# Kernel tuning notes

Hardware: AMD Instinct MI355X
Metric: run time of the kernel (lower is better)

The kernel has to match this reference:

```python
import jax, jax.numpy as jnp
import numpy as np

EPSILON = 0.01            # params.epsilon (cluster precision regularizer)
GAMMA = 0.005             # params.gamma (outlier/uniform component weight)
FIX_CLUSTER_POS_ITER = 1  # params.fix_cluster_pos_iter


def _sqdist(TVs, X):
    # TVs: (M, 3, N) transformed points, X: (K, 3) cluster means -> (M, N, K)
    return ((TVs ** 2).sum(1)[:, :, None]
            + (X ** 2).sum(1)[None, None, :]
            - 2.0 * jnp.einsum('mdn,kd->mnk', TVs, X))


def setup_inputs() -> dict:
    key = jax.random.key(0)
    kV, kX, kQ = jax.random.split(key, 3)
    M, N, K = 8, 8192, 256
    Vs = jax.random.normal(kV, (M, 3, N), dtype=jnp.float32)      # 3D point clouds
    X0 = jax.random.normal(kX, (K, 3), dtype=jnp.float32)         # init cluster means (sphere init)
    Q0 = 0.1 + 0.2 * jax.random.uniform(kQ, (K,), dtype=jnp.float32)  # init cluster precisions
    return {"Vs": Vs, "X0": X0, "Q0": Q0, "num_iters": 6}


def reference(Vs, X0, Q0, num_iters):
    M, _, N = Vs.shape
    K = X0.shape[0]
    dtype = Vs.dtype

    # mean_init: init_R = I, init_t = -mean(V) per view
    t0 = -Vs.mean(axis=2, keepdims=True)          # (M, 3, 1)
    TVs = Vs + t0
    beta = GAMMA * jnp.mean(Q0) ** 1.5            # get_default_beta(Q, gamma)

    X, Q = X0, Q0
    ds = _sqdist(TVs, X)                          # (M, N, K)
    R = jnp.broadcast_to(jnp.eye(3, dtype=dtype), (M, 3, 3))
    t = t0[:, :, 0]

    for i in range(num_iters):
        if i != num_iters - 1:  # detach everything except backprop_iter = [last]
            X = jax.lax.stop_gradient(X)
            Q = jax.lax.stop_gradient(Q)
            ds = jax.lax.stop_gradient(ds)

        # E-step: soft posteriors with uniform outlier component beta
        ap = jnp.exp(-0.5 * ds * Q) * Q ** 1.5    # (M, N, K); priors = 1, pyz_feature = 1
        a = ap / (ap.sum(axis=-1, keepdims=True) + beta)

        # M-step: weighted sufficient statistics
        L = a.sum(axis=1)                                   # (M, K)
        W = jnp.einsum('mdn,mnk->mdk', Vs, a) * Q           # (M, 3, K)
        mW = W.sum(axis=-1)                                 # (M, 3)
        b = L * Q                                           # (M, K)
        mX = jnp.einsum('mk,kd->md', b, X)                  # (M, 3)
        z = b.sum(axis=-1)                                  # (M,)

        # P = (W @ X)^T - mX mW^T / z  : 3x3 weighted cross-covariance per view
        P = (jnp.einsum('mdk,ke->med', W, X)
             - mX[:, :, None] * mW[:, None, :] / z[:, None, None])

        # batched Procrustes: R = U diag(1,1,det(U V^T)) V^T
        U, _, Vt = jnp.linalg.svd(P)
        det = jnp.linalg.det(jnp.einsum('mij,mjk->mik', U, Vt))
        sgn = jnp.concatenate([jnp.ones((M, 2), dtype), det[:, None]], axis=1)
        R = jnp.einsum('mij,mjk->mik', U * sgn[:, None, :], Vt)   # (M, 3, 3)
        t = (mX - jnp.einsum('mij,mj->mi', R, mW)) / z[:, None]   # (M, 3)
        TVs = jnp.einsum('mij,mjn->min', R, Vs) + t[:, :, None]   # (M, 3, N)

        # shared cluster updates (sum over views)
        den = L.sum(axis=0)                                 # (K,)
        if i > FIX_CLUSTER_POS_ITER:
            X = jnp.einsum('mdn,mnk->kd', TVs, a) / den[:, None]
        ds = _sqdist(TVs, X)
        wn = (a * ds).sum(axis=(0, 1))                      # (K,)
        Q = 3.0 * den / (wn + 3.0 * den * EPSILON)

    return TVs, R, t, X
```

## Files before the change

### kernel.cpp

```cpp
#include <hip/hip_runtime.h>
#include <math.h>

#define Mv 8
#define Nv 8192
#define Kv 256
#define BPM 32
#define NBLK (Mv*BPM)
#define NPB (Nv/BPM)
#define NITER 6
#define EPSILON_C 0.01f
#define GAMMA_C 0.005f

#define WS_R     0
#define WS_T     72
#define WS_X     96
#define WS_Q     864
#define WS_BETA  1120
#define WS_ACC   1124
#define AC_STATS 0
#define AC_L     128
#define AC_W     2176
#define AC_H     8320
#define ACCSZ    10368

__device__ __forceinline__ float wave_red_sum(float x) {
  int v;
  float t;
  v = __builtin_bit_cast(int, x);
  t = __builtin_bit_cast(float, __builtin_amdgcn_update_dpp(0, v, 0x111, 0xf, 0xf, true));
  x += t; v = __builtin_bit_cast(int, x);
  t = __builtin_bit_cast(float, __builtin_amdgcn_update_dpp(0, v, 0x112, 0xf, 0xf, true));
  x += t; v = __builtin_bit_cast(int, x);
  t = __builtin_bit_cast(float, __builtin_amdgcn_update_dpp(0, v, 0x114, 0xf, 0xf, true));
  x += t; v = __builtin_bit_cast(int, x);
  t = __builtin_bit_cast(float, __builtin_amdgcn_update_dpp(0, v, 0x118, 0xf, 0xf, true));
  x += t; v = __builtin_bit_cast(int, x);
  t = __builtin_bit_cast(float, __builtin_amdgcn_update_dpp(0, v, 0x142, 0xa, 0xf, false));
  x += t; v = __builtin_bit_cast(int, x);
  t = __builtin_bit_cast(float, __builtin_amdgcn_update_dpp(0, v, 0x143, 0xc, 0xf, false));
  x += t;
  return __builtin_bit_cast(float, __builtin_amdgcn_readlane(__builtin_bit_cast(int, x), 63));
}

__global__ __launch_bounds__(256) void p0_init(const float* __restrict__ Vs,
                                               const float* __restrict__ X0,
                                               const float* __restrict__ Q0,
                                               float* __restrict__ ws) {
  __shared__ float sred[4];
  int tid = threadIdx.x;
  int b = blockIdx.x;
  int wave = tid >> 6, lane = tid & 63;
  if (b < 24) {
    int m = b / 3, d = b % 3;
    const float* src = Vs + (size_t)(m*3 + d) * Nv;
    float s = 0.f;
    for (int n = tid; n < Nv; n += 256) s += src[n];
    s = wave_red_sum(s);
    if (lane == 0) sred[wave] = s;
    __syncthreads();
    if (tid == 0) {
      float tot = sred[0]+sred[1]+sred[2]+sred[3];
      ws[WS_T + m*3 + d] = -tot / (float)Nv;
    }
    if (d == 0 && tid < 9) {
      ws[WS_R + m*9 + tid] = (tid==0||tid==4||tid==8) ? 1.f : 0.f;
    }
  } else {
    float s = (tid < Kv) ? Q0[tid] : 0.f;
    s = wave_red_sum(s);
    if (lane == 0) sred[wave] = s;
    __syncthreads();
    if (tid == 0) {
      float mq = (sred[0]+sred[1]+sred[2]+sred[3]) / (float)Kv;
      ws[WS_BETA] = GAMMA_C * mq * sqrtf(mq);
    }
    if (tid < Kv) ws[WS_Q + tid] = Q0[tid];
    for (int i = tid; i < Kv*3; i += 256) ws[WS_X + i] = X0[i];
    for (int i = tid; i < ACCSZ; i += 256) ws[WS_ACC + i] = 0.f;
  }
}

#define JROTF(app,aqq,apq,apr,aqr, vp0,vp1,vp2, vq0,vq1,vq2) do {           \
    float tau_ = (aqq - app) * __builtin_amdgcn_rcpf(2.0f*apq);             \
    float tt_ = __builtin_amdgcn_rcpf(fabsf(tau_) +                         \
                   __builtin_amdgcn_sqrtf(fmaf(tau_,tau_,1.0f)));           \
    tt_ = (tau_ < 0.0f) ? -tt_ : tt_;                                       \
    tt_ = (apq == 0.0f) ? 0.0f : tt_;                                       \
    float c_ = __builtin_amdgcn_rsqf(fmaf(tt_,tt_,1.0f)), s_ = tt_*c_;      \
    float papq_ = apq;                                                      \
    app = fmaf(-tt_,papq_,app); aqq = fmaf(tt_,papq_,aqq); apq = 0.0f;      \
    float tp_ = apr, tq_ = aqr;                                             \
    apr = c_*tp_ - s_*tq_; aqr = s_*tp_ + c_*tq_;                           \
    tp_=vp0; tq_=vq0; vp0=c_*tp_-s_*tq_; vq0=s_*tp_+c_*tq_;                 \
    tp_=vp1; tq_=vq1; vp1=c_*tp_-s_*tq_; vq1=s_*tp_+c_*tq_;                 \
    tp_=vp2; tq_=vq2; vp2=c_*tp_-s_*tq_; vq2=s_*tp_+c_*tq_;                 \
  } while(0)

#define CSWAP3F(la,lb, a0,a1,a2, b0,b1,b2) do {                             \
    if (la < lb) { float t_;                                                \
      t_=la; la=lb; lb=t_; t_=a0; a0=b0; b0=t_;                             \
      t_=a1; a1=b1; b1=t_; t_=a2; a2=b2; b2=t_; }                           \
  } while(0)

template<int ITPREV>
__device__ __forceinline__ void small_update(const float* __restrict__ acc,
                                             const float* __restrict__ ws,
                                             int tid,
                                             float (*sX)[3], float* sQ,
                                             float (*sR)[9], float (*sT)[3],
                                             float* sTn) {
  const int k = tid;
  float lk[Mv], w0v[Mv], w1v[Mv], w2v[Mv], hk[Mv];
  #pragma unroll
  for (int mm=0;mm<Mv;mm++) {
    lk[mm]  = acc[AC_L + mm*Kv + k];
    w0v[mm] = acc[AC_W + (mm*3+0)*Kv + k];
    w1v[mm] = acc[AC_W + (mm*3+1)*Kv + k];
    w2v[mm] = acc[AC_W + (mm*3+2)*Kv + k];
    hk[mm]  = acc[AC_H + mm*Kv + k];
  }
  float xp0 = 0.f, xp1 = 0.f, xp2 = 0.f;
  if (ITPREV <= 1) {
    xp0 = ws[WS_X + k*3+0]; xp1 = ws[WS_X + k*3+1]; xp2 = ws[WS_X + k*3+2];
  }

  if (tid < Mv) {
    int mm = tid;
    const float* st = acc + AC_STATS + mm*16;
    float s0=st[0], s1=st[1], s2v=st[2], s3=st[3], s4=st[4], s5=st[5],
          s6=st[6], s7=st[7], s8=st[8], s9=st[9], s10=st[10], s11=st[11],
          s12=st[12], s13=st[13], s14=st[14], s15=st[15];
    float z = s0;
    float mX0 = s1, mX1 = s2v, mX2 = s3;
    float mW0 = s4, mW1 = s5, mW2 = s6;
    float iz = __builtin_amdgcn_rcpf(z);
    float P00 = s7  - mX0*mW0*iz;
    float P01 = s8  - mX0*mW1*iz;
    float P02 = s9  - mX0*mW2*iz;
    float P10 = s10 - mX1*mW0*iz;
    float P11 = s11 - mX1*mW1*iz;
    float P12 = s12 - mX1*mW2*iz;
    float P20 = s13 - mX2*mW0*iz;
    float P21 = s14 - mX2*mW1*iz;
    float P22 = s15 - mX2*mW2*iz;
    float a00 = P00*P00 + P10*P10 + P20*P20;
    float a01 = P00*P01 + P10*P11 + P20*P21;
    float a02 = P00*P02 + P10*P12 + P20*P22;
    float a11 = P01*P01 + P11*P11 + P21*P21;
    float a12 = P01*P02 + P11*P12 + P21*P22;
    float a22 = P02*P02 + P12*P12 + P22*P22;
    float v00=1, v01=0, v02=0, v10=0, v11=1, v12=0, v20=0, v21=0, v22=1;
    #pragma unroll 1
    for (int sweep = 0; sweep < 8; sweep++) {
      JROTF(a00,a11,a01, a02,a12, v00,v10,v20, v01,v11,v21);
      JROTF(a00,a22,a02, a01,a12, v00,v10,v20, v02,v12,v22);
      JROTF(a11,a22,a12, a01,a02, v01,v11,v21, v02,v12,v22);
    }
    float l0 = a00, l1 = a11, l2 = a22;
    CSWAP3F(l0,l1, v00,v10,v20, v01,v11,v21);
    CSWAP3F(l1,l2, v01,v11,v21, v02,v12,v22);
    CSWAP3F(l0,l1, v00,v10,v20, v01,v11,v21);
    float detP = P00*(P11*P22-P12*P21) - P01*(P10*P22-P12*P20)
               + P02*(P10*P21-P11*P20);
    float s2d = (detP < 0.0f) ? -1.0f : 1.0f;
    float tiny = 1e-18f*l0 + 1e-30f;
    float w0i = __builtin_amdgcn_rsqf(fmaxf(l0,tiny));
    float w1i = __builtin_amdgcn_rsqf(fmaxf(l1,tiny));
    float w2i = s2d*__builtin_amdgcn_rsqf(fmaxf(l2,tiny));
    float M00 = w0i*v00*v00 + w1i*v01*v01 + w2i*v02*v02;
    float M01 = w0i*v00*v10 + w1i*v01*v11 + w2i*v02*v12;
    float M02 = w0i*v00*v20 + w1i*v01*v21 + w2i*v02*v22;
    float M11 = w0i*v10*v10 + w1i*v11*v11 + w2i*v12*v12;
    float M12 = w0i*v10*v20 + w1i*v11*v21 + w2i*v12*v22;
    float M22 = w0i*v20*v20 + w1i*v21*v21 + w2i*v22*v22;
    float R00n = P00*M00 + P01*M01 + P02*M02;
    float R01n = P00*M01 + P01*M11 + P02*M12;
    float R02n = P00*M02 + P01*M12 + P02*M22;
    float R10n = P10*M00 + P11*M01 + P12*M02;
    float R11n = P10*M01 + P11*M11 + P12*M12;
    float R12n = P10*M02 + P11*M12 + P12*M22;
    float R20n = P20*M00 + P21*M01 + P22*M02;
    float R21n = P20*M01 + P21*M11 + P22*M12;
    float R22n = P20*M02 + P21*M12 + P22*M22;
    float tm0 = (mX0 - (R00n*mW0 + R01n*mW1 + R02n*mW2))*iz;
    float tm1 = (mX1 - (R10n*mW0 + R11n*mW1 + R12n*mW2))*iz;
    float tm2 = (mX2 - (R20n*mW0 + R21n*mW1 + R22n*mW2))*iz;
    sR[mm][0]=R00n; sR[mm][1]=R01n; sR[mm][2]=R02n;
    sR[mm][3]=R10n; sR[mm][4]=R11n; sR[mm][5]=R12n;
    sR[mm][6]=R20n; sR[mm][7]=R21n; sR[mm][8]=R22n;
    sT[mm][0]=tm0; sT[mm][1]=tm1; sT[mm][2]=tm2;
    sTn[mm] = tm0*tm0 + tm1*tm1 + tm2*tm2;
  }
  __syncthreads();
  {
    float den = 0.f, Xn0=0.f, Xn1=0.f, Xn2=0.f, S2=0.f;
    #pragma unroll
    for (int mm=0;mm<Mv;mm++) {
      float r0 = sR[mm][0]*w0v[mm] + sR[mm][1]*w1v[mm] + sR[mm][2]*w2v[mm];
      float r1 = sR[mm][3]*w0v[mm] + sR[mm][4]*w1v[mm] + sR[mm][5]*w2v[mm];
      float r2 = sR[mm][6]*w0v[mm] + sR[mm][7]*w1v[mm] + sR[mm][8]*w2v[mm];
      float tt0 = sT[mm][0], tt1 = sT[mm][1], tt2 = sT[mm][2];
      den += lk[mm];
      Xn0 += r0 + tt0*lk[mm]; Xn1 += r1 + tt1*lk[mm]; Xn2 += r2 + tt2*lk[mm];
      S2  += hk[mm] + 2.f*(tt0*r0+tt1*r1+tt2*r2) + sTn[mm]*lk[mm];
    }
    float x0, x1, x2;
    if (ITPREV > 1) { float inv = __builtin_amdgcn_rcpf(den);
                      x0=Xn0*inv; x1=Xn1*inv; x2=Xn2*inv; }
    else            { x0=xp0; x1=xp1; x2=xp2; }
    float wn = S2 + (x0*x0+x1*x1+x2*x2)*den - 2.f*(x0*Xn0+x1*Xn1+x2*Xn2);
    float qn = 3.f*den / (wn + 3.f*den*EPSILON_C);
    sX[k][0]=x0; sX[k][1]=x1; sX[k][2]=x2;
    sQ[k] = qn;
  }
}

template<int IT>
__global__ __launch_bounds__(256) void p_iter(const float* __restrict__ Vs,
                                              float* __restrict__ ws) {
  __shared__ __align__(16) float sC[Kv][8];
  __shared__ __align__(16) float sPT[NPB][4];
  __shared__ __align__(16) float sVV[NPB][4];
  __shared__ float sInv[NPB];
  __shared__ float st4[4][16];
  __shared__ float sX[Kv][3];
  __shared__ float sQ[Kv];
  __shared__ float sR[Mv][9];
  __shared__ float sT[Mv][3];
  __shared__ float sTn[Mv];

  int tid  = threadIdx.x;
  int wave = tid >> 6, lane = tid & 63;
  int bid  = blockIdx.x;
  int m    = bid / BPM;
  int blk  = bid % BPM;
  int n0   = blk * NPB;

  float* acc  = ws + WS_ACC + (IT % 3)*ACCSZ;
  float* accz = ws + WS_ACC + ((IT+1) % 3)*ACCSZ;
  float beta = ws[WS_BETA];

  if (IT == 0) {
    if (tid < 72) ((float*)sR)[tid] = ws[WS_R + tid];
    if (tid < 24) ((float*)sT)[tid] = ws[WS_T + tid];
    sX[tid][0] = ws[WS_X + 3*tid+0];
    sX[tid][1] = ws[WS_X + 3*tid+1];
    sX[tid][2] = ws[WS_X + 3*tid+2];
    sQ[tid]    = ws[WS_Q + tid];
  } else {
    const float* accp = ws + WS_ACC + ((IT+2) % 3)*ACCSZ;
    small_update<(IT > 0) ? (IT-1) : 0>(accp, ws, tid, sX, sQ, sR, sT, sTn);
  }
  __syncthreads();

  { int base = bid*41;
    if (tid < 41 && base + tid < ACCSZ) accz[base + tid] = 0.f; }

  const float L2E = 1.4426950408889634f;
  float xx = sX[tid][0], xy = sX[tid][1], xz = sX[tid][2];
  float q  = sQ[tid];
  float qL   = q * L2E;
  float kA   = -0.5f*qL;
  float kXx  = qL*xx, kXy = qL*xy, kXz = qL*xz;
  float kB   = kA*(xx*xx+xy*xy+xz*xz);
  float kQ32 = q*sqrtf(q);
  sC[tid][0]=kXx; sC[tid][1]=kXy; sC[tid][2]=kXz;
  sC[tid][3]=kA;  sC[tid][4]=kB;  sC[tid][5]=kQ32;

  float R00=sR[m][0],R01=sR[m][1],R02=sR[m][2];
  float R10=sR[m][3],R11=sR[m][4],R12=sR[m][5];
  float R20=sR[m][6],R21=sR[m][7],R22=sR[m][8];
  float t0=sT[m][0], t1=sT[m][1], t2=sT[m][2];
  int n = n0 + tid;
  float vx = Vs[(size_t)(m*3+0)*Nv + n];
  float vy = Vs[(size_t)(m*3+1)*Nv + n];
  float vz = Vs[(size_t)(m*3+2)*Nv + n];
  float px = fmaf(R00,vx, fmaf(R01,vy, fmaf(R02,vz, t0)));
  float py = fmaf(R10,vx, fmaf(R11,vy, fmaf(R12,vz, t1)));
  float pz = fmaf(R20,vx, fmaf(R21,vy, fmaf(R22,vz, t2)));
  float tvn = fmaf(px,px, fmaf(py,py, pz*pz));
  float vn  = fmaf(vx,vx, fmaf(vy,vy, vz*vz));
  sPT[tid][0]=px; sPT[tid][1]=py; sPT[tid][2]=pz; sPT[tid][3]=tvn;
  sVV[tid][0]=vx; sVV[tid][1]=vy; sVV[tid][2]=vz; sVV[tid][3]=vn;
  __syncthreads();

  {
    float s0=0.f, s1=0.f, s2=0.f, s3=0.f;
    #pragma unroll 2
    for (int k = 0; k < Kv; k += 4) {
      float4 c0 = *reinterpret_cast<const float4*>(&sC[k+0][0]);
      float2 d0 = *reinterpret_cast<const float2*>(&sC[k+0][4]);
      float4 c1 = *reinterpret_cast<const float4*>(&sC[k+1][0]);
      float2 d1 = *reinterpret_cast<const float2*>(&sC[k+1][4]);
      float4 c2 = *reinterpret_cast<const float4*>(&sC[k+2][0]);
      float2 d2 = *reinterpret_cast<const float2*>(&sC[k+2][4]);
      float4 c3 = *reinterpret_cast<const float4*>(&sC[k+3][0]);
      float2 d3 = *reinterpret_cast<const float2*>(&sC[k+3][4]);
      float a0 = fmaf(px,c0.x, fmaf(py,c0.y, fmaf(pz,c0.z, fmaf(c0.w,tvn,d0.x))));
      float a1 = fmaf(px,c1.x, fmaf(py,c1.y, fmaf(pz,c1.z, fmaf(c1.w,tvn,d1.x))));
      float a2 = fmaf(px,c2.x, fmaf(py,c2.y, fmaf(pz,c2.z, fmaf(c2.w,tvn,d2.x))));
      float a3 = fmaf(px,c3.x, fmaf(py,c3.y, fmaf(pz,c3.z, fmaf(c3.w,tvn,d3.x))));
      s0 = fmaf(__builtin_amdgcn_exp2f(a0), d0.y, s0);
      s1 = fmaf(__builtin_amdgcn_exp2f(a1), d1.y, s1);
      s2 = fmaf(__builtin_amdgcn_exp2f(a2), d2.y, s2);
      s3 = fmaf(__builtin_amdgcn_exp2f(a3), d3.y, s3);
    }
    sInv[tid] = __builtin_amdgcn_rcpf(((s0+s1)+(s2+s3)) + beta);
  }
  __syncthreads();

  float aL=0.f, aWx=0.f, aWy=0.f, aWz=0.f, aH=0.f;
  #pragma unroll 4
  for (int nn = 0; nn < NPB; nn++) {
    float4 p = *reinterpret_cast<const float4*>(&sPT[nn][0]);
    float4 v = *reinterpret_cast<const float4*>(&sVV[nn][0]);
    float iv = sInv[nn];
    float arg = fmaf(kXx,p.x, fmaf(kXy,p.y, fmaf(kXz,p.z, fmaf(kA,p.w,kB))));
    float a = __builtin_amdgcn_exp2f(arg) * (kQ32*iv);
    aL += a;
    aWx = fmaf(a,v.x,aWx);
    aWy = fmaf(a,v.y,aWy);
    aWz = fmaf(a,v.z,aWz);
    aH  = fmaf(a,v.w,aH);
  }
  atomicAdd(&acc[AC_L + m*Kv + tid], aL);
  atomicAdd(&acc[AC_W + (m*3+0)*Kv + tid], aWx);
  atomicAdd(&acc[AC_W + (m*3+1)*Kv + tid], aWy);
  atomicAdd(&acc[AC_W + (m*3+2)*Kv + tid], aWz);
  atomicAdd(&acc[AC_H + m*Kv + tid], aH);

  {
    float bk = aL*q;
    float sw0 = aWx*q, sw1 = aWy*q, sw2 = aWz*q;
    float pr[16];
    pr[0]=bk;  pr[1]=bk*xx; pr[2]=bk*xy; pr[3]=bk*xz;
    pr[4]=sw0; pr[5]=sw1;   pr[6]=sw2;
    pr[7]=sw0*xx;  pr[8]=sw1*xx;  pr[9]=sw2*xx;
    pr[10]=sw0*xy; pr[11]=sw1*xy; pr[12]=sw2*xy;
    pr[13]=sw0*xz; pr[14]=sw1*xz; pr[15]=sw2*xz;
    float red[16];
    #pragma unroll
    for (int v2=0; v2<16; v2++) red[v2] = wave_red_sum(pr[v2]);
    if (lane == 0) {
      #pragma unroll
      for (int v2=0; v2<16; v2++) st4[wave][v2] = red[v2];
    }
    __syncthreads();
    if (tid < 16)
      atomicAdd(&acc[AC_STATS + m*16 + ((tid + blk) & 15)],
                st4[0][(tid+blk)&15]+st4[1][(tid+blk)&15]+
                st4[2][(tid+blk)&15]+st4[3][(tid+blk)&15]);
  }
}

#define OUT_TOTAL (Mv*3*Nv + 72 + 24 + Kv*3)
__global__ __launch_bounds__(256) void p3_final(const float* __restrict__ Vs,
                                                const float* __restrict__ ws,
                                                float* __restrict__ out) {
  __shared__ float sX[Kv][3];
  __shared__ float sQ[Kv];
  __shared__ float sR[Mv][9];
  __shared__ float sT[Mv][3];
  __shared__ float sTn[Mv];
  int tid = threadIdx.x;
  const float* acc = ws + WS_ACC + ((NITER-1) % 3)*ACCSZ;
  small_update<NITER-1>(acc, ws, tid, sX, sQ, sR, sT, sTn);
  __syncthreads();

  for (int idx = blockIdx.x*256 + tid; idx < OUT_TOTAL; idx += 256*256) {
    if (idx < Mv*3*Nv) {
      int m = idx / (3*Nv);
      int r = idx % (3*Nv);
      int d = r / Nv;
      int n = r % Nv;
      float vx = Vs[(size_t)(m*3+0)*Nv + n];
      float vy = Vs[(size_t)(m*3+1)*Nv + n];
      float vz = Vs[(size_t)(m*3+2)*Nv + n];
      out[idx] = fmaf(sR[m][d*3+0],vx,
                 fmaf(sR[m][d*3+1],vy,
                 fmaf(sR[m][d*3+2],vz, sT[m][d])));
    } else {
      int j = idx - Mv*3*Nv;
      float v;
      if (j < 72)      v = ((float*)sR)[j];
      else if (j < 96) v = ((float*)sT)[j-72];
      else             v = ((float*)sX)[j-96];
      out[idx] = v;
    }
  }
}

extern "C" void kernel_launch(void* const* d_in, const int* in_sizes, int n_in,
                              void* d_out, int out_size, void* d_ws, size_t ws_size,
                              hipStream_t stream) {
  const float* Vs = (const float*)d_in[0];
  const float* X0 = (const float*)d_in[1];
  const float* Q0 = (const float*)d_in[2];
  float* out = (float*)d_out;
  float* ws  = (float*)d_ws;

  p0_init<<<25, 256, 0, stream>>>(Vs, X0, Q0, ws);
  p_iter<0><<<NBLK, 256, 0, stream>>>(Vs, ws);
  p_iter<1><<<NBLK, 256, 0, stream>>>(Vs, ws);
  p_iter<2><<<NBLK, 256, 0, stream>>>(Vs, ws);
  p_iter<3><<<NBLK, 256, 0, stream>>>(Vs, ws);
  p_iter<4><<<NBLK, 256, 0, stream>>>(Vs, ws);
  p_iter<5><<<NBLK, 256, 0, stream>>>(Vs, ws);
  p3_final<<<256, 256, 0, stream>>>(Vs, ws, out);
}
```

Measured before the change: 207.7 us.

## Register-tile E-step over 4 clusters per thread and double blocks per view

Doubles blocks per view so each block handles 128 points. Both passes are register-tiled: the normaliser pass has each thread compute two points over a quarter of the clusters, and the stats pass has each thread hold four clusters' constants over a quarter of the points. Partials are combined with quad DPP reductions. The per-point normaliser is folded into the exponent as -log2(sum+beta), and a cluster's exp(kB)·q^1.5 is precomputed, removing multiplies from the inner loops. Swizzled LDS layouts cut bank conflicts, at the cost of more blocks, more global atomics and extra register pressure.

```diff
diff --git a/kernel.cpp b/kernel.cpp
--- a/kernel.cpp
+++ b/kernel.cpp
@@ -4,12 +4,15 @@
 #define Mv 8
 #define Nv 8192
 #define Kv 256
-#define BPM 32
+#define BPM 64
 #define NBLK (Mv*BPM)
 #define NPB (Nv/BPM)
 #define NITER 6
 #define EPSILON_C 0.01f
 #define GAMMA_C 0.005f
+
+#define SWZK(k) ((((k)&63)<<2)|((k)>>6))
+#define SWZP(p) ((((p)&31)<<2)|((p)>>5))
 
 #define WS_R     0
 #define WS_T     72
@@ -40,6 +43,23 @@
   t = __builtin_bit_cast(float, __builtin_amdgcn_update_dpp(0, v, 0x143, 0xc, 0xf, false));
   x += t;
   return __builtin_bit_cast(float, __builtin_amdgcn_readlane(__builtin_bit_cast(int, x), 63));
+}
+
+__device__ __forceinline__ float quad_red_sum(float x) {
+  int v = __builtin_bit_cast(int, x);
+  float t = __builtin_bit_cast(float, __builtin_amdgcn_update_dpp(0, v, 0xB1, 0xf, 0xf, true));
+  x += t; v = __builtin_bit_cast(int, x);
+  t = __builtin_bit_cast(float, __builtin_amdgcn_update_dpp(0, v, 0x4E, 0xf, 0xf, true));
+  x += t;
+  return x;
+}
+
+__device__ __forceinline__ float sel4(int c, float a0, float a1, float a2, float a3) {
+  float r = a0;
+  r = (c==1) ? a1 : r;
+  r = (c==2) ? a2 : r;
+  r = (c==3) ? a3 : r;
+  return r;
 }
 
 __global__ __launch_bounds__(256) void p0_init(const float* __restrict__ Vs,
@@ -218,10 +238,11 @@
 template<int IT>
 __global__ __launch_bounds__(256) void p_iter(const float* __restrict__ Vs,
                                               float* __restrict__ ws) {
-  __shared__ __align__(16) float sC[Kv][8];
-  __shared__ __align__(16) float sPT[NPB][4];
-  __shared__ __align__(16) float sVV[NPB][4];
-  __shared__ float sInv[NPB];
+  __shared__ __align__(16) float sC4[Kv][4];
+  __shared__ float sKC[Kv];
+  __shared__ __align__(16) float sP4[NPB][4];
+  __shared__ __align__(16) float sV4[NPB][4];
+  __shared__ float sLi[NPB];
   __shared__ float st4[4][16];
   __shared__ float sX[Kv][3];
   __shared__ float sQ[Kv];
@@ -253,91 +274,125 @@
   }
   __syncthreads();
 
-  { int base = bid*41;
-    if (tid < 41 && base + tid < ACCSZ) accz[base + tid] = 0.f; }
+  { int base = bid*21;
+    if (tid < 21 && base + tid < ACCSZ) accz[base + tid] = 0.f; }
 
   const float L2E = 1.4426950408889634f;
-  float xx = sX[tid][0], xy = sX[tid][1], xz = sX[tid][2];
-  float q  = sQ[tid];
-  float qL   = q * L2E;
-  float kA   = -0.5f*qL;
-  float kXx  = qL*xx, kXy = qL*xy, kXz = qL*xz;
-  float kB   = kA*(xx*xx+xy*xy+xz*xz);
-  float kQ32 = q*sqrtf(q);
-  sC[tid][0]=kXx; sC[tid][1]=kXy; sC[tid][2]=kXz;
-  sC[tid][3]=kA;  sC[tid][4]=kB;  sC[tid][5]=kQ32;
-
-  float R00=sR[m][0],R01=sR[m][1],R02=sR[m][2];
-  float R10=sR[m][3],R11=sR[m][4],R12=sR[m][5];
-  float R20=sR[m][6],R21=sR[m][7],R22=sR[m][8];
-  float t0=sT[m][0], t1=sT[m][1], t2=sT[m][2];
-  int n = n0 + tid;
-  float vx = Vs[(size_t)(m*3+0)*Nv + n];
-  float vy = Vs[(size_t)(m*3+1)*Nv + n];
-  float vz = Vs[(size_t)(m*3+2)*Nv + n];
-  float px = fmaf(R00,vx, fmaf(R01,vy, fmaf(R02,vz, t0)));
-  float py = fmaf(R10,vx, fmaf(R11,vy, fmaf(R12,vz, t1)));
-  float pz = fmaf(R20,vx, fmaf(R21,vy, fmaf(R22,vz, t2)));
-  float tvn = fmaf(px,px, fmaf(py,py, pz*pz));
-  float vn  = fmaf(vx,vx, fmaf(vy,vy, vz*vz));
-  sPT[tid][0]=px; sPT[tid][1]=py; sPT[tid][2]=pz; sPT[tid][3]=tvn;
-  sVV[tid][0]=vx; sVV[tid][1]=vy; sVV[tid][2]=vz; sVV[tid][3]=vn;
+  {
+    float xx = sX[tid][0], xy = sX[tid][1], xz = sX[tid][2];
+    float q  = sQ[tid];
+    float qL = q * L2E;
+    float kA = -0.5f*qL;
+    float kB = kA*(xx*xx+xy*xy+xz*xz);
+    float kQ32 = q*sqrtf(q);
+    int rr = SWZK(tid);
+    *reinterpret_cast<float4*>(&sC4[rr][0]) = make_float4(qL*xx, qL*xy, qL*xz, kA);
+    sKC[rr] = kQ32 * __builtin_amdgcn_exp2f(kB);
+  }
+  if (tid < NPB) {
+    float R00=sR[m][0],R01=sR[m][1],R02=sR[m][2];
+    float R10=sR[m][3],R11=sR[m][4],R12=sR[m][5];
+    float R20=sR[m][6],R21=sR[m][7],R22=sR[m][8];
+    float t0=sT[m][0], t1=sT[m][1], t2=sT[m][2];
+    int n = n0 + tid;
+    float vx = Vs[(size_t)(m*3+0)*Nv + n];
+    float vy = Vs[(size_t)(m*3+1)*Nv + n];
+    float vz = Vs[(size_t)(m*3+2)*Nv + n];
+    float px = fmaf(R00,vx, fmaf(R01,vy, fmaf(R02,vz, t0)));
+    float py = fmaf(R10,vx, fmaf(R11,vy, fmaf(R12,vz, t1)));
+    float pz = fmaf(R20,vx, fmaf(R21,vy, fmaf(R22,vz, t2)));
+    float tvn = fmaf(px,px, fmaf(py,py, pz*pz));
+    float vn  = fmaf(vx,vx, fmaf(vy,vy, vz*vz));
+    int pr = SWZP(tid);
+    *reinterpret_cast<float4*>(&sP4[pr][0]) = make_float4(px,py,pz,tvn);
+    *reinterpret_cast<float4*>(&sV4[pr][0]) = make_float4(vx,vy,vz,vn);
+  }
   __syncthreads();
 
   {
-    float s0=0.f, s1=0.f, s2=0.f, s3=0.f;
-    #pragma unroll 2
-    for (int k = 0; k < Kv; k += 4) {
-      float4 c0 = *reinterpret_cast<const float4*>(&sC[k+0][0]);
-      float2 d0 = *reinterpret_cast<const float2*>(&sC[k+0][4]);
-      float4 c1 = *reinterpret_cast<const float4*>(&sC[k+1][0]);
-      float2 d1 = *reinterpret_cast<const float2*>(&sC[k+1][4]);
-      float4 c2 = *reinterpret_cast<const float4*>(&sC[k+2][0]);
-      float2 d2 = *reinterpret_cast<const float2*>(&sC[k+2][4]);
-      float4 c3 = *reinterpret_cast<const float4*>(&sC[k+3][0]);
-      float2 d3 = *reinterpret_cast<const float2*>(&sC[k+3][4]);
-      float a0 = fmaf(px,c0.x, fmaf(py,c0.y, fmaf(pz,c0.z, fmaf(c0.w,tvn,d0.x))));
-      float a1 = fmaf(px,c1.x, fmaf(py,c1.y, fmaf(pz,c1.z, fmaf(c1.w,tvn,d1.x))));
-      float a2 = fmaf(px,c2.x, fmaf(py,c2.y, fmaf(pz,c2.z, fmaf(c2.w,tvn,d2.x))));
-      float a3 = fmaf(px,c3.x, fmaf(py,c3.y, fmaf(pz,c3.z, fmaf(c3.w,tvn,d3.x))));
-      s0 = fmaf(__builtin_amdgcn_exp2f(a0), d0.y, s0);
-      s1 = fmaf(__builtin_amdgcn_exp2f(a1), d1.y, s1);
-      s2 = fmaf(__builtin_amdgcn_exp2f(a2), d2.y, s2);
-      s3 = fmaf(__builtin_amdgcn_exp2f(a3), d3.y, s3);
-    }
-    sInv[tid] = __builtin_amdgcn_rcpf(((s0+s1)+(s2+s3)) + beta);
+    int ks = tid & 3, pg = tid >> 2;
+    float4 P0 = *reinterpret_cast<const float4*>(&sP4[SWZP(2*pg+0)][0]);
+    float4 P1 = *reinterpret_cast<const float4*>(&sP4[SWZP(2*pg+1)][0]);
+    float s0 = 0.f, s1 = 0.f;
+    #pragma unroll 4
+    for (int j = 0; j < Kv/4; j++) {
+      int row = (j<<2) | ks;
+      float4 c4 = *reinterpret_cast<const float4*>(&sC4[row][0]);
+      float kc = sKC[row];
+      float a0 = fmaf(P0.x,c4.x, fmaf(P0.y,c4.y, fmaf(P0.z,c4.z, P0.w*c4.w)));
+      float a1 = fmaf(P1.x,c4.x, fmaf(P1.y,c4.y, fmaf(P1.z,c4.z, P1.w*c4.w)));
+      s0 = fmaf(__builtin_amdgcn_exp2f(a0), kc, s0);
+      s1 = fmaf(__builtin_amdgcn_exp2f(a1), kc, s1);
+    }
+    float S0 = quad_red_sum(s0);
+    float S1 = quad_red_sum(s1);
+    if (ks < 2) {
+      float Ssel = (ks == 1) ? S1 : S0;
+      sLi[SWZP(2*pg + ks)] = -__log2f(Ssel + beta);
+    }
   }
   __syncthreads();
 
-  float aL=0.f, aWx=0.f, aWy=0.f, aWz=0.f, aH=0.f;
-  #pragma unroll 4
-  for (int nn = 0; nn < NPB; nn++) {
-    float4 p = *reinterpret_cast<const float4*>(&sPT[nn][0]);
-    float4 v = *reinterpret_cast<const float4*>(&sVV[nn][0]);
-    float iv = sInv[nn];
-    float arg = fmaf(kXx,p.x, fmaf(kXy,p.y, fmaf(kXz,p.z, fmaf(kA,p.w,kB))));
-    float a = __builtin_amdgcn_exp2f(arg) * (kQ32*iv);
-    aL += a;
-    aWx = fmaf(a,v.x,aWx);
-    aWy = fmaf(a,v.y,aWy);
-    aWz = fmaf(a,v.z,aWz);
-    aH  = fmaf(a,v.w,aH);
-  }
-  atomicAdd(&acc[AC_L + m*Kv + tid], aL);
-  atomicAdd(&acc[AC_W + (m*3+0)*Kv + tid], aWx);
-  atomicAdd(&acc[AC_W + (m*3+1)*Kv + tid], aWy);
-  atomicAdd(&acc[AC_W + (m*3+2)*Kv + tid], aWz);
-  atomicAdd(&acc[AC_H + m*Kv + tid], aH);
-
-  {
-    float bk = aL*q;
-    float sw0 = aWx*q, sw1 = aWy*q, sw2 = aWz*q;
+  float cXx0,cXy0,cXz0,cA0,cC0, cXx1,cXy1,cXz1,cA1,cC1,
+        cXx2,cXy2,cXz2,cA2,cC2, cXx3,cXy3,cXz3,cA3,cC3;
+  {
+    int kg = tid >> 2;
+    #define LDC(c) { int rr = SWZK(4*kg + c); \
+      float4 t4 = *reinterpret_cast<const float4*>(&sC4[rr][0]); \
+      cXx##c=t4.x; cXy##c=t4.y; cXz##c=t4.z; cA##c=t4.w; cC##c=sKC[rr]; }
+    LDC(0) LDC(1) LDC(2) LDC(3)
+    #undef LDC
+  }
+  float L0=0,L1=0,L2=0,L3=0, Wx0=0,Wx1=0,Wx2=0,Wx3=0,
+        Wy0=0,Wy1=0,Wy2=0,Wy3=0, Wz0=0,Wz1=0,Wz2=0,Wz3=0,
+        H0=0,H1=0,H2=0,H3=0;
+  {
+    int ns = tid & 3;
+    #pragma unroll 4
+    for (int j = 0; j < NPB/4; j++) {
+      int prow = (j<<2) | ns;
+      float4 p4 = *reinterpret_cast<const float4*>(&sP4[prow][0]);
+      float4 v4 = *reinterpret_cast<const float4*>(&sV4[prow][0]);
+      float li = sLi[prow];
+      #define P2K(c) { \
+        float arg = fmaf(p4.w, cA##c, li); \
+        arg = fmaf(p4.x, cXx##c, fmaf(p4.y, cXy##c, fmaf(p4.z, cXz##c, arg))); \
+        float e = __builtin_amdgcn_exp2f(arg) * cC##c; \
+        L##c += e; \
+        Wx##c = fmaf(e, v4.x, Wx##c); Wy##c = fmaf(e, v4.y, Wy##c); \
+        Wz##c = fmaf(e, v4.z, Wz##c); H##c  = fmaf(e, v4.w, H##c); }
+      P2K(0) P2K(1) P2K(2) P2K(3)
+      #undef P2K
+    }
+  }
+  L0=quad_red_sum(L0); L1=quad_red_sum(L1); L2=quad_red_sum(L2); L3=quad_red_sum(L3);
+  Wx0=quad_red_sum(Wx0); Wx1=quad_red_sum(Wx1); Wx2=quad_red_sum(Wx2); Wx3=quad_red_sum(Wx3);
+  Wy0=quad_red_sum(Wy0); Wy1=quad_red_sum(Wy1); Wy2=quad_red_sum(Wy2); Wy3=quad_red_sum(Wy3);
+  Wz0=quad_red_sum(Wz0); Wz1=quad_red_sum(Wz1); Wz2=quad_red_sum(Wz2); Wz3=quad_red_sum(Wz3);
+  H0=quad_red_sum(H0); H1=quad_red_sum(H1); H2=quad_red_sum(H2); H3=quad_red_sum(H3);
+  int c = tid & 3;
+  float vL  = sel4(c, L0,L1,L2,L3);
+  float vWx = sel4(c, Wx0,Wx1,Wx2,Wx3);
+  float vWy = sel4(c, Wy0,Wy1,Wy2,Wy3);
+  float vWz = sel4(c, Wz0,Wz1,Wz2,Wz3);
+  float vH  = sel4(c, H0,H1,H2,H3);
+  atomicAdd(&acc[AC_L + m*Kv + tid], vL);
+  atomicAdd(&acc[AC_W + (m*3+0)*Kv + tid], vWx);
+  atomicAdd(&acc[AC_W + (m*3+1)*Kv + tid], vWy);
+  atomicAdd(&acc[AC_W + (m*3+2)*Kv + tid], vWz);
+  atomicAdd(&acc[AC_H + m*Kv + tid], vH);
+
+  {
+    float q  = sQ[tid];
+    float x0 = sX[tid][0], x1 = sX[tid][1], x2 = sX[tid][2];
+    float bk = vL*q;
+    float sw0 = vWx*q, sw1 = vWy*q, sw2 = vWz*q;
     float pr[16];
-    pr[0]=bk;  pr[1]=bk*xx; pr[2]=bk*xy; pr[3]=bk*xz;
+    pr[0]=bk;  pr[1]=bk*x0; pr[2]=bk*x1; pr[3]=bk*x2;
     pr[4]=sw0; pr[5]=sw1;   pr[6]=sw2;
-    pr[7]=sw0*xx;  pr[8]=sw1*xx;  pr[9]=sw2*xx;
-    pr[10]=sw0*xy; pr[11]=sw1*xy; pr[12]=sw2*xy;
-    pr[13]=sw0*xz; pr[14]=sw1*xz; pr[15]=sw2*xz;
+    pr[7]=sw0*x0;  pr[8]=sw1*x0;  pr[9]=sw2*x0;
+    pr[10]=sw0*x1; pr[11]=sw1*x1; pr[12]=sw2*x1;
+    pr[13]=sw0*x2; pr[14]=sw1*x2; pr[15]=sw2*x2;
     float red[16];
     #pragma unroll
     for (int v2=0; v2<16; v2++) red[v2] = wave_red_sum(pr[v2]);
```

Result: faster. 183.6 us (-11.6%).
